# Kernel tuning notes

Hardware: AMD Instinct MI355X
Metric: run time of the kernel (lower is better)

## Reference

```python
import jax, jax.numpy as jnp
import numpy as np
from jax import lax

B, T, H, E, V = 1000, 101, 256, 256, 64


def _lstm(x, Wih, Whh, bih, bhh):
    # x: [B, T, D_in]; PyTorch gate order i, f, g, o. Initial hidden/cell are zeros.
    Bx = x.shape[0]
    Hh = Whh.shape[1]
    b = bih + bhh
    h0 = jnp.zeros((Bx, Hh), x.dtype)
    c0 = jnp.zeros((Bx, Hh), x.dtype)

    def step(carry, xt):
        h, c = carry
        g = xt @ Wih.T + h @ Whh.T + b  # [B, 4H]
        i, f, gg, o = jnp.split(g, 4, axis=-1)
        c = jax.nn.sigmoid(f) * c + jax.nn.sigmoid(i) * jnp.tanh(gg)
        h = jax.nn.sigmoid(o) * jnp.tanh(c)
        return (h, c), h

    _, hs = lax.scan(step, (h0, c0), jnp.swapaxes(x, 0, 1))  # hs: [T, B, H]
    return jnp.swapaxes(hs, 0, 1)


def setup_inputs():
    key = jax.random.key(0)
    ks = jax.random.split(key, 20)
    n = lambda k, s: jax.random.normal(k, s, jnp.float32) * 0.05
    return {
        'input_ids': jax.random.randint(ks[0], (B, T), 0, V, dtype=jnp.int32),
        'emb': n(ks[1], (V, E)),
        'Wih1': n(ks[2], (4 * H, E)), 'Whh1': n(ks[3], (4 * H, H)),
        'bih1': n(ks[4], (4 * H,)), 'bhh1': n(ks[5], (4 * H,)),
        'Wih2': n(ks[6], (4 * H, H)), 'Whh2': n(ks[7], (4 * H, H)),
        'bih2': n(ks[8], (4 * H,)), 'bhh2': n(ks[9], (4 * H,)),
        'Wattn': n(ks[10], (T, H, H)), 'battn': n(ks[11], (T, H)),
        'W1': n(ks[12], (512, H * T)), 'b1': n(ks[13], (512,)),
        'W2': n(ks[14], (128, 512)), 'b2': n(ks[15], (128,)),
        'W3': n(ks[16], (64, 128)), 'b3': n(ks[17], (64,)),
        'Wout': n(ks[18], (1, 64)), 'bout': n(ks[19], (1,)),
    }


def reference(input_ids, emb, Wih1, Whh1, bih1, bhh1, Wih2, Whh2, bih2, bhh2,
              Wattn, battn, W1, b1, W2, b2, W3, b3, Wout, bout):
    x = emb[input_ids]                                    # [B, T, E]
    h1 = _lstm(x, Wih1, Whh1, bih1, bhh1)                 # [B, T, H]
    h2 = _lstm(h1, Wih2, Whh2, bih2, bhh2)                # [B, T, H]
    # per-timestep Linear (the 101-call loop in torch), fused as one batched GEMM
    attn = jnp.einsum('bth,tkh->btk', h2, Wattn) + battn  # y_t = h_t @ W_t.T + b_t
    w = jax.nn.softmax(attn, axis=2)                      # softmax over feature dim
    applied = w * x                                       # [B, T, E]
    flat = applied.reshape(applied.shape[0], -1)          # [B, T*E]
    d = jax.nn.relu(flat @ W1.T + b1)
    d = jax.nn.relu(d @ W2.T + b2)
    d = jax.nn.relu(d @ W3.T + b3)
    tag = d @ Wout.T + bout                               # [B, 1]
    return tag, applied
```

## Files before the change

kernel.cpp:

```cpp
#include <hip/hip_runtime.h>
#include <hip/hip_bf16.h>


#define B_    1000
#define T_    101
#define E_    256
#define H_    256
#define BPAD  1008
#define MPAD  101824
#define NG    1024
#define NSLICE 63

typedef __bf16 bf16;
typedef __bf16 bf16x8 __attribute__((ext_vector_type(8)));
typedef float  f32x4  __attribute__((ext_vector_type(4)));

__device__ __forceinline__ bf16 f2b(float f){
  unsigned u = __builtin_bit_cast(unsigned, f);
  u += 0x7FFFu + ((u >> 16) & 1u);
  unsigned short h = (unsigned short)(u >> 16);
  return __builtin_bit_cast(bf16, h);
}
__device__ __forceinline__ unsigned packbf(float a, float b){
  unsigned ua = __builtin_bit_cast(unsigned, a);
  ua += 0x7FFFu + ((ua >> 16) & 1u);
  unsigned ub = __builtin_bit_cast(unsigned, b);
  ub += 0x7FFFu + ((ub >> 16) & 1u);
  return (ua >> 16) | (ub & 0xffff0000u);
}
__device__ __forceinline__ float sigm(float x){ return 1.f/(1.f + __expf(-x)); }
__device__ __forceinline__ float tanh_(float x){ return 2.f/(1.f + __expf(-2.f*x)) - 1.f; }

__global__ void pack_bT(const float* __restrict__ src, bf16* __restrict__ dst,
                        int N, int K)
{
  const long batch = blockIdx.y;
  src += batch * (long)N * K;
  dst += batch * (long)(K/32) * N * 32;
  const int tid = blockIdx.x * blockDim.x + threadIdx.x;
  const int total = (K/32) * N * 4;
  if (tid >= total) return;
  const int kkc = tid & 3;
  const int rem = tid >> 2;
  const int n = rem % N;
  const int q = rem / N;
  const float* s = src + (long)n*K + q*32 + kkc*8;
  bf16x8 v;
  #pragma unroll
  for (int e=0;e<8;e++) v[e] = f2b(s[e]);
  *reinterpret_cast<bf16x8*>(dst + ((long)q*N + n)*32 + kkc*8) = v;
}

__global__ void tr_f32(const float* __restrict__ src, float* __restrict__ dst,
                       int N, int K)
{
  const int id = blockIdx.x * blockDim.x + threadIdx.x;
  if (id >= N*K) return;
  const int k = id / N, j = id % N;
  dst[(long)k*N + j] = src[(long)j*K + k];
}

__global__ void bias_sum(const float* __restrict__ a, const float* __restrict__ b,
                         float* __restrict__ o, int n)
{
  const int i = blockIdx.x * blockDim.x + threadIdx.x;
  if (i < n) o[i] = a[i] + b[i];
}

__global__ void embed_k(const int* __restrict__ ids, const float* __restrict__ emb,
                        bf16* __restrict__ x)
{
  const int tid = blockIdx.x * blockDim.x + threadIdx.x;
  const int m = tid >> 5;
  const int c = (tid & 31) << 3;
  bf16x8 v;
  if (m < B_*T_) {
    const int id = ids[m];
    const float* e = emb + (long)id*E_ + c;
    #pragma unroll
    for (int j=0;j<8;j++) v[j] = f2b(e[j]);
  } else {
    #pragma unroll
    for (int j=0;j<8;j++) v[j] = f2b(0.f);
  }
  *reinterpret_cast<bf16x8*>(x + (long)m*256 + c) = v;
}

#define MF(a,b,c) __builtin_amdgcn_mfma_f32_16x16x32_bf16((a),(b),(c),0,0,0)
#define LDW(q_,off_)  (*reinterpret_cast<const bf16x8*>(bbW + ((long)(q_)*NG + (off_))*32))
#define LDX8(q_,off_) (*reinterpret_cast<const bf16x8*>(bbX + ((long)(q_)*NG + (off_))*32))

#define XK_ALL() { \
  bf16x8 xA0 = LDX8(0,0), xA1 = LDX8(0,16), xB0, xB1; \
  _Pragma("unroll") \
  for (int h2x=0; h2x<4; ++h2x){ \
    const int q0x = 2*h2x; \
    xB0 = LDX8(q0x+1,0); xB1 = LDX8(q0x+1,16); \
    { bf16x8 ax = *reinterpret_cast<const bf16x8*>(&xbuf[l16*264 + q0x*32 + lg*8]); \
      acc0 = MF(ax,xA0,acc0); acc1 = MF(ax,xA1,acc1); } \
    if (q0x+2 < 8){ xA0 = LDX8(q0x+2,0); xA1 = LDX8(q0x+2,16); } \
    { bf16x8 ax = *reinterpret_cast<const bf16x8*>(&xbuf[l16*264 + (q0x+1)*32 + lg*8]); \
      acc0 = MF(ax,xB0,acc0); acc1 = MF(ax,xB1,acc1); } \
  } }

__launch_bounds__(512, 1)
__global__ void lstm_v4(const bf16* __restrict__ X, const bf16* __restrict__ Wihp,
                        const bf16* __restrict__ Whhp, const float* __restrict__ bias,
                        bf16* __restrict__ Hout, unsigned* __restrict__ hX,
                        unsigned* __restrict__ flags)
{
  __shared__ __align__(16) bf16 hbuf[16*264];
  __shared__ __align__(16) bf16 xbuf[16*264];
  __shared__ float gstage[256*17];
  const int bid = blockIdx.x;
  const int s = bid >> 2, g = bid & 3;
  const int b0 = s * 16;
  const int tid = threadIdx.x;
  const int wave = tid >> 6, lane = tid & 63;
  const int l16 = lane & 15, lg = lane >> 4;
  const int qd  = wave >> 1;
  const int h32 = (wave & 1) * 32;

  const bf16* bbW = Whhp + ((long)(qd*256 + g*64 + h32 + l16) * 32 + lg*8);
  const bf16* bbX = Wihp + ((long)(qd*256 + g*64 + h32 + l16) * 32 + lg*8);

  const int row = tid >> 5;
  const int k32 = tid & 31;
  const int j2  = k32 * 2;
  float c0 = 0.f, c1 = 0.f;

  const long grow = (long)(b0 + row) * T_;
  const bf16* xp  = X    + grow*256 + k32*8;
  bf16*       hop = Hout + grow*256 + g*64 + j2;

  const float bvi0 = bias[      g*64 + j2    ];
  const float bvi1 = bias[      g*64 + j2 + 1];
  const float bvf0 = bias[256 + g*64 + j2    ];
  const float bvf1 = bias[256 + g*64 + j2 + 1];
  const float bvg0 = bias[512 + g*64 + j2    ];
  const float bvg1 = bias[512 + g*64 + j2 + 1];
  const float bvo0 = bias[768 + g*64 + j2    ];
  const float bvo1 = bias[768 + g*64 + j2 + 1];

  unsigned* flag = flags + s*16;
  unsigned* hx0 = hX + (size_t)s*2048 + row*128 + g*32 + k32;
  unsigned* hx1 = hx0 + (size_t)NSLICE*2048;
  const unsigned* rb0 = hX + (size_t)s*2048 + row*128;
  const unsigned* rb1 = rb0 + (size_t)NSLICE*2048;

  const int qo0 = 2*g, qo1 = 2*g + 1;

  for (int i = tid; i < 16*264; i += 512) hbuf[i] = f2b(0.f);
  *reinterpret_cast<bf16x8*>(&xbuf[row*264 + k32*8]) =
      *reinterpret_cast<const bf16x8*>(xp);
  __syncthreads();

  bf16x8 f0[6], f1[6];
  #pragma unroll
  for (int i=0;i<6;++i){
    const int qn = (qo0 + 2 + i) & 7;
    f0[i] = LDW(qn, 0);
    f1[i] = LDW(qn, 16);
  }
  const bf16x8 o00 = LDW(qo0, 0), o01 = LDW(qo0, 16);
  const bf16x8 o10 = LDW(qo1, 0), o11 = LDW(qo1, 16);

  f32x4 acc0 = {0.f,0.f,0.f,0.f}, acc1 = {0.f,0.f,0.f,0.f};
  XK_ALL();

  for (int t = 0; t < T_; ++t){
    const bf16x8 xreg = *reinterpret_cast<const bf16x8*>(xp + (long)(t+1)*256);

    #pragma unroll
    for (int i = 0; i < 6; ++i){
      const int qi = (qo0 + 2 + i) & 7;
      bf16x8 a = *reinterpret_cast<const bf16x8*>(&hbuf[l16*264 + qi*32 + lg*8]);
      acc0 = MF(a, f0[i], acc0);
      acc1 = MF(a, f1[i], acc1);
    }
    {
      const int jj = wave*32 + l16;
      float* gc0 = &gstage[jj*17 + lg*4];
      gc0[0]=acc0[0]; gc0[1]=acc0[1]; gc0[2]=acc0[2]; gc0[3]=acc0[3];
      float* gc1 = &gstage[(jj+16)*17 + lg*4];
      gc1[0]=acc1[0]; gc1[1]=acc1[1]; gc1[2]=acc1[2]; gc1[3]=acc1[3];
    }
    __syncthreads();

    const float i0 = sigm (bvi0 + gstage[(j2      )*17 + row]);
    const float i1 = sigm (bvi1 + gstage[(j2 +   1)*17 + row]);
    const float f0e= sigm (bvf0 + gstage[(j2 +  64)*17 + row]);
    const float f1e= sigm (bvf1 + gstage[(j2 +  65)*17 + row]);
    const float g0e= tanh_(bvg0 + gstage[(j2 + 128)*17 + row]);
    const float g1e= tanh_(bvg1 + gstage[(j2 + 129)*17 + row]);
    const float o0 = sigm (bvo0 + gstage[(j2 + 192)*17 + row]);
    const float o1 = sigm (bvo1 + gstage[(j2 + 193)*17 + row]);
    c0 = f0e*c0 + i0*g0e;
    c1 = f1e*c1 + i1*g1e;
    const unsigned hw = packbf(o0*tanh_(c0), o1*tanh_(c1));

    *reinterpret_cast<unsigned*>(&hbuf[row*264 + g*64 + j2]) = hw;
    *reinterpret_cast<bf16x8*>(&xbuf[row*264 + k32*8]) = xreg;
    __hip_atomic_store((t&1) ? hx1 : hx0, hw, __ATOMIC_RELAXED, __HIP_MEMORY_SCOPE_AGENT);

    __syncthreads();
    if (tid == 0)
      __hip_atomic_fetch_add(flag, 1u, __ATOMIC_RELAXED, __HIP_MEMORY_SCOPE_AGENT);

    *reinterpret_cast<unsigned*>(hop + (long)t*256) = hw;

    {
      acc0 = f32x4{0.f,0.f,0.f,0.f};
      acc1 = f32x4{0.f,0.f,0.f,0.f};
      bf16x8 a0 = *reinterpret_cast<const bf16x8*>(&hbuf[l16*264 + qo0*32 + lg*8]);
      acc0 = MF(a0, o00, acc0); acc1 = MF(a0, o01, acc1);
      bf16x8 a1 = *reinterpret_cast<const bf16x8*>(&hbuf[l16*264 + qo1*32 + lg*8]);
      acc0 = MF(a1, o10, acc0); acc1 = MF(a1, o11, acc1);
      XK_ALL();
    }

    {
      const unsigned tgt = 4u*(t+1);
      if (lane == 0){
        int guard = 0;
        while (__hip_atomic_load(flag, __ATOMIC_RELAXED, __HIP_MEMORY_SCOPE_AGENT) < tgt
               && ++guard < (1<<20))
          __builtin_amdgcn_s_sleep(1);
      }
      asm volatile("" ::: "memory");
      __builtin_amdgcn_sched_barrier(0);
      const unsigned* rb = (t&1) ? rb1 : rb0;
      #pragma unroll
      for (int sb=1; sb<4; ++sb){
        const int g2 = (g + sb) & 3;
        const unsigned w = __hip_atomic_load(rb + g2*32 + k32,
                                             __ATOMIC_RELAXED, __HIP_MEMORY_SCOPE_AGENT);
        *reinterpret_cast<unsigned*>(&hbuf[row*264 + g2*64 + j2]) = w;
      }
    }
    __syncthreads();
  }
}

__launch_bounds__(256)
__global__ void attn_applied(const bf16* __restrict__ H2, const bf16* __restrict__ Wap,
                             const float* __restrict__ battn, const int* __restrict__ ids,
                             const float* __restrict__ emb, float* __restrict__ applied,
                             bf16* __restrict__ flat)
{
  __shared__ __align__(16) bf16 albuf[32*264];
  __shared__ float sbuf[32*257];
  const int mt = blockIdx.x, t = blockIdx.y;
  const int b0 = mt*32;
  const int tid = threadIdx.x;
  const int wave = tid >> 6, lane = tid & 63;
  const int l16 = lane & 15, lg = lane >> 4;

  for (int i = tid; i < 1024; i += 256){
    const int r = i >> 5, cc = (i & 31) << 3;
    const int b = b0 + r;
    bf16x8 v;
    if (b < B_) v = *reinterpret_cast<const bf16x8*>(H2 + ((long)b*T_ + t)*256 + cc);
    else { 
      #pragma unroll
      for (int j=0;j<8;j++) v[j] = f2b(0.f);
    }
    *reinterpret_cast<bf16x8*>(&albuf[r*264 + cc]) = v;
  }
  __syncthreads();

  f32x4 acc[2][4];
  #pragma unroll
  for (int ms=0; ms<2; ++ms)
    #pragma unroll
    for (int ns=0; ns<4; ++ns) acc[ms][ns] = f32x4{0.f,0.f,0.f,0.f};

  const bf16* bb = Wap + (long)t*65536 + ((long)(wave*64 + l16) * 32 + lg*8);
  #pragma unroll 2
  for (int q=0; q<8; ++q){
    bf16x8 a0 = *reinterpret_cast<const bf16x8*>(&albuf[l16*264 + q*32 + lg*8]);
    bf16x8 a1 = *reinterpret_cast<const bf16x8*>(&albuf[(16 + l16)*264 + q*32 + lg*8]);
    #pragma unroll
    for (int ns=0; ns<4; ++ns){
      bf16x8 b = *reinterpret_cast<const bf16x8*>(bb + ((long)q*256 + ns*16) * 32);
      acc[0][ns] = __builtin_amdgcn_mfma_f32_16x16x32_bf16(a0, b, acc[0][ns], 0,0,0);
      acc[1][ns] = __builtin_amdgcn_mfma_f32_16x16x32_bf16(a1, b, acc[1][ns], 0,0,0);
    }
  }
  float bv[4];
  #pragma unroll
  for (int ns=0; ns<4; ++ns) bv[ns] = battn[t*256 + wave*64 + ns*16 + l16];
  #pragma unroll
  for (int ms=0; ms<2; ++ms)
    #pragma unroll
    for (int ns=0; ns<4; ++ns)
      #pragma unroll
      for (int r=0; r<4; ++r)
        sbuf[(ms*16 + lg*4 + r)*257 + wave*64 + ns*16 + l16] = acc[ms][ns][r] + bv[ns];
  __syncthreads();

  const int row = tid >> 3, seg = tid & 7;
  const float* srow = &sbuf[row*257 + seg*32];
  float v[32];
  float mx = -1e30f;
  #pragma unroll
  for (int i=0;i<32;++i){ v[i] = srow[i]; mx = fmaxf(mx, v[i]); }
  #pragma unroll
  for (int off=1; off<8; off<<=1) mx = fmaxf(mx, __shfl_xor(mx, off));
  float s = 0.f;
  #pragma unroll
  for (int i=0;i<32;++i){ v[i] = __expf(v[i] - mx); s += v[i]; }
  #pragma unroll
  for (int off=1; off<8; off<<=1) s += __shfl_xor(s, off);
  const float inv = 1.f / s;
  const int b = b0 + row;
  if (b < B_){
    const int id = ids[b*T_ + t];
    const float* ex = emb + (long)id*256 + seg*32;
    float* ap = applied + ((long)b*T_ + t)*256 + seg*32;
    bf16* fp = flat + (long)b*25856 + t*256 + seg*32;
    #pragma unroll
    for (int i=0;i<32;++i){
      const float val = v[i]*inv*ex[i];
      ap[i] = val;
      fp[i] = f2b(val);
    }
  }
}

__launch_bounds__(512)
__global__ void gemm_mlp1(const bf16* __restrict__ A, const bf16* __restrict__ Bp,
                          float* __restrict__ part)
{
  const int m0 = blockIdx.x * 32;
  const int ks = blockIdx.y;
  const int tid = threadIdx.x;
  const int wave = tid >> 6, lane = tid & 63;
  const int l16 = lane & 15, lg = lane >> 4;
  f32x4 acc[2][4];
  #pragma unroll
  for (int ms=0; ms<2; ++ms)
    #pragma unroll
    for (int ns=0; ns<4; ++ns) acc[ms][ns] = f32x4{0.f,0.f,0.f,0.f};

  const bf16* arow0 = A + (long)(m0 + l16)*25856 + lg*8;
  const bf16* arow1 = A + (long)(m0 + 16 + l16)*25856 + lg*8;
  const bf16* bb = Bp + ((long)(wave*64 + l16) * 32 + lg*8);
  #pragma unroll 2
  for (int q = ks*101; q < ks*101 + 101; ++q){
    bf16x8 a0 = *reinterpret_cast<const bf16x8*>(arow0 + (long)q*32);
    bf16x8 a1 = *reinterpret_cast<const bf16x8*>(arow1 + (long)q*32);
    #pragma unroll
    for (int ns=0; ns<4; ++ns){
      bf16x8 b = *reinterpret_cast<const bf16x8*>(bb + ((long)q*512 + ns*16) * 32);
      acc[0][ns] = __builtin_amdgcn_mfma_f32_16x16x32_bf16(a0, b, acc[0][ns], 0,0,0);
      acc[1][ns] = __builtin_amdgcn_mfma_f32_16x16x32_bf16(a1, b, acc[1][ns], 0,0,0);
    }
  }
  #pragma unroll
  for (int ms=0; ms<2; ++ms)
    #pragma unroll
    for (int ns=0; ns<4; ++ns)
      #pragma unroll
      for (int r=0; r<4; ++r)
        part[((long)ks*1024 + m0 + ms*16 + lg*4 + r)*512 + wave*64 + ns*16 + l16] = acc[ms][ns][r];
}

__global__ void reduce_relu(const float* __restrict__ part, const float* __restrict__ b1,
                            float* __restrict__ d1)
{
  const int idx = blockIdx.x*256 + threadIdx.x;
  const int n = idx & 511, m = idx >> 9;
  float s = b1[n];
  #pragma unroll
  for (int k=0;k<8;k++) s += part[((long)k*1024 + m)*512 + n];
  d1[idx] = fmaxf(s, 0.f);
}

__launch_bounds__(128)
__global__ void mlp_tail(const float* __restrict__ d1, const float* __restrict__ W2T,
                         const float* __restrict__ b2, const float* __restrict__ W3T,
                         const float* __restrict__ b3, const float* __restrict__ Wout,
                         const float* __restrict__ bout, float* __restrict__ tag)
{
  __shared__ float r1[512];
  __shared__ float r2[128];
  __shared__ float r3[64];
  const int b = blockIdx.x;
  const int tid = threadIdx.x;
  for (int i = tid; i < 512; i += 128) r1[i] = d1[(long)b*512 + i];
  __syncthreads();
  float a = b2[tid];
  #pragma unroll 8
  for (int k=0;k<512;++k) a += W2T[k*128 + tid] * r1[k];
  r2[tid] = fmaxf(a, 0.f);
  __syncthreads();
  if (tid < 64){
    float a3 = b3[tid];
    #pragma unroll 8
    for (int k=0;k<128;++k) a3 += W3T[k*64 + tid] * r2[k];
    r3[tid] = fmaxf(a3, 0.f);
  }
  __syncthreads();
  if (tid < 64){
    float p = r3[tid] * Wout[tid];
    #pragma unroll
    for (int off=1; off<64; off<<=1) p += __shfl_xor(p, off);
    if (tid == 0) tag[b] = p + bout[0];
  }
}

extern "C" void kernel_launch(void* const* d_in, const int* in_sizes, int n_in,
                              void* d_out, int out_size, void* d_ws, size_t ws_size,
                              hipStream_t stream)
{
  const int*   ids   = (const int*)  d_in[0];
  const float* emb   = (const float*)d_in[1];
  const float* Wih1  = (const float*)d_in[2];
  const float* Whh1  = (const float*)d_in[3];
  const float* bih1  = (const float*)d_in[4];
  const float* bhh1  = (const float*)d_in[5];
  const float* Wih2  = (const float*)d_in[6];
  const float* Whh2  = (const float*)d_in[7];
  const float* bih2  = (const float*)d_in[8];
  const float* bhh2  = (const float*)d_in[9];
  const float* Wattn = (const float*)d_in[10];
  const float* battn = (const float*)d_in[11];
  const float* W1    = (const float*)d_in[12];
  const float* b1    = (const float*)d_in[13];
  const float* W2    = (const float*)d_in[14];
  const float* b2    = (const float*)d_in[15];
  const float* W3    = (const float*)d_in[16];
  const float* b3    = (const float*)d_in[17];
  const float* Wout  = (const float*)d_in[18];
  const float* bout  = (const float*)d_in[19];
  float* out = (float*)d_out;
  char*  ws  = (char*)d_ws;

  constexpr size_t OW_IH1 = 0;
  constexpr size_t OW_HH1 = 524288;
  constexpr size_t OW_IH2 = 1048576;
  constexpr size_t OW_HH2 = 1572864;
  constexpr size_t OW_ATT = 2097152;
  constexpr size_t OW_W1  = 15335424;
  constexpr size_t OW_W2T = 41811968;
  constexpr size_t OW_W3T = 42074112;
  constexpr size_t OB1    = 42106880;
  constexpr size_t OB2    = 42110976;
  constexpr size_t OXH2   = 42115072;
  constexpr size_t OG     = 94248960;
  constexpr size_t OFLAT  = OG;
  constexpr size_t OPART  = OG + 52953088;
  constexpr size_t OH1    = 302784512;
  constexpr size_t OD1    = 354918400;
  constexpr size_t OHX    = OD1;
  constexpr size_t OFLG   = OD1 + 1032192;
  constexpr size_t NEED   = 357015552;
  if (ws_size < NEED) return;

  bf16*  pIH1 = (bf16*) (ws + OW_IH1);
  bf16*  pHH1 = (bf16*) (ws + OW_HH1);
  bf16*  pIH2 = (bf16*) (ws + OW_IH2);
  bf16*  pHH2 = (bf16*) (ws + OW_HH2);
  bf16*  pATT = (bf16*) (ws + OW_ATT);
  bf16*  pW1  = (bf16*) (ws + OW_W1);
  float* pW2T = (float*)(ws + OW_W2T);
  float* pW3T = (float*)(ws + OW_W3T);
  float* pB1  = (float*)(ws + OB1);
  float* pB2  = (float*)(ws + OB2);
  bf16*  pXH2 = (bf16*) (ws + OXH2);
  bf16*  pFLAT= (bf16*) (ws + OFLAT);
  float* pPART= (float*)(ws + OPART);
  bf16*  pH1  = (bf16*) (ws + OH1);
  float* pD1  = (float*)(ws + OD1);
  unsigned* pHX  = (unsigned*)(ws + OHX);
  unsigned* pFL1 = (unsigned*)(ws + OFLG);
  unsigned* pFL2 = (unsigned*)(ws + OFLG + 4096);

  hipMemsetAsync(ws + OFLG, 0, 8192, stream);
  hipMemsetAsync(ws + OFLAT + (size_t)B_*25856*2, 0, (size_t)24*25856*2, stream);

  pack_bT<<<dim3(128),        256, 0, stream>>>(Wih1,  pIH1, 1024, 256);
  pack_bT<<<dim3(128),        256, 0, stream>>>(Whh1,  pHH1, 1024, 256);
  pack_bT<<<dim3(128),        256, 0, stream>>>(Wih2,  pIH2, 1024, 256);
  pack_bT<<<dim3(128),        256, 0, stream>>>(Whh2,  pHH2, 1024, 256);
  pack_bT<<<dim3(32, 101),    256, 0, stream>>>(Wattn, pATT, 256,  256);
  pack_bT<<<dim3(6464),       256, 0, stream>>>(W1,    pW1,  512,  25856);
  tr_f32 <<<dim3(256),        256, 0, stream>>>(W2, pW2T, 128, 512);
  tr_f32 <<<dim3(32),         256, 0, stream>>>(W3, pW3T, 64, 128);
  bias_sum<<<dim3(4),         256, 0, stream>>>(bih1, bhh1, pB1, 1024);
  bias_sum<<<dim3(4),         256, 0, stream>>>(bih2, bhh2, pB2, 1024);

  embed_k<<<dim3(12728), 256, 0, stream>>>(ids, emb, pXH2);

  lstm_v4<<<dim3(252), 512, 0, stream>>>(pXH2, pIH1, pHH1, pB1, pH1,  pHX, pFL1);
  lstm_v4<<<dim3(252), 512, 0, stream>>>(pH1,  pIH2, pHH2, pB2, pXH2, pHX, pFL2);

  attn_applied<<<dim3(32, 101), 256, 0, stream>>>(pXH2, pATT, battn, ids, emb,
                                                  out + 1000, pFLAT);

  gemm_mlp1  <<<dim3(32, 8), 512, 0, stream>>>(pFLAT, pW1, pPART);
  reduce_relu<<<dim3(2048),  256, 0, stream>>>(pPART, b1, pD1);
  mlp_tail   <<<dim3(1000),  128, 0, stream>>>(pD1, pW2T, b2, pW3T, b3, Wout, bout, out);
}
```

Measured before the change: 870.2 us.

## Use per-group step flags in LSTM, reload weights per step, remap grids for XCD locality

The LSTM's single atomic counter per batch slice, bumped by fetch_add, becomes four per-group flags, each written with a plain atomic store and polled together, so the atomic read-modify-write on a shared counter goes away. The own-slice Whh fragments and the f0/f1 weight registers are now reloaded from global memory every step instead of held for the whole kernel, which lowers register pressure but adds a load per step. The attn_applied and gemm_mlp1 launches switch to 1D grids whose block index is decoded so blocks that share data land on the same XCD, aiming for better L2 reuse. The extra per-step weight loads could lengthen the serial LSTM critical path.

```diff
diff --git a/kernel.cpp b/kernel.cpp
--- a/kernel.cpp
+++ b/kernel.cpp
@@ -104,7 +104,7 @@
   } }
 
 __launch_bounds__(512, 1)
-__global__ void lstm_v4(const bf16* __restrict__ X, const bf16* __restrict__ Wihp,
+__global__ void lstm_v5(const bf16* __restrict__ X, const bf16* __restrict__ Wihp,
                         const bf16* __restrict__ Whhp, const float* __restrict__ bias,
                         bf16* __restrict__ Hout, unsigned* __restrict__ hX,
                         unsigned* __restrict__ flags)
@@ -142,7 +142,7 @@
   const float bvo0 = bias[768 + g*64 + j2    ];
   const float bvo1 = bias[768 + g*64 + j2 + 1];
 
-  unsigned* flag = flags + s*16;
+  unsigned* flagw = flags + s*16;
   unsigned* hx0 = hX + (size_t)s*2048 + row*128 + g*32 + k32;
   unsigned* hx1 = hx0 + (size_t)NSLICE*2048;
   const unsigned* rb0 = hX + (size_t)s*2048 + row*128;
@@ -162,8 +162,6 @@
     f0[i] = LDW(qn, 0);
     f1[i] = LDW(qn, 16);
   }
-  const bf16x8 o00 = LDW(qo0, 0), o01 = LDW(qo0, 16);
-  const bf16x8 o10 = LDW(qo1, 0), o11 = LDW(qo1, 16);
 
   f32x4 acc0 = {0.f,0.f,0.f,0.f}, acc1 = {0.f,0.f,0.f,0.f};
   XK_ALL();
@@ -205,11 +203,14 @@
 
     __syncthreads();
     if (tid == 0)
-      __hip_atomic_fetch_add(flag, 1u, __ATOMIC_RELAXED, __HIP_MEMORY_SCOPE_AGENT);
+      __hip_atomic_store(flagw + g, (unsigned)(t+1),
+                         __ATOMIC_RELAXED, __HIP_MEMORY_SCOPE_AGENT);
 
     *reinterpret_cast<unsigned*>(hop + (long)t*256) = hw;
 
     {
+      bf16x8 o00 = LDW(qo0, 0), o01 = LDW(qo0, 16);
+      bf16x8 o10 = LDW(qo1, 0), o11 = LDW(qo1, 16);
       acc0 = f32x4{0.f,0.f,0.f,0.f};
       acc1 = f32x4{0.f,0.f,0.f,0.f};
       bf16x8 a0 = *reinterpret_cast<const bf16x8*>(&hbuf[l16*264 + qo0*32 + lg*8]);
@@ -217,15 +218,27 @@
       bf16x8 a1 = *reinterpret_cast<const bf16x8*>(&hbuf[l16*264 + qo1*32 + lg*8]);
       acc0 = MF(a1, o10, acc0); acc1 = MF(a1, o11, acc1);
       XK_ALL();
+      #pragma unroll
+      for (int i=0;i<6;++i){
+        const int qn = (qo0 + 2 + i) & 7;
+        f0[i] = LDW(qn, 0);
+        f1[i] = LDW(qn, 16);
+      }
     }
 
     {
-      const unsigned tgt = 4u*(t+1);
+      const unsigned tgt = (unsigned)(t+1);
       if (lane == 0){
         int guard = 0;
-        while (__hip_atomic_load(flag, __ATOMIC_RELAXED, __HIP_MEMORY_SCOPE_AGENT) < tgt
-               && ++guard < (1<<20))
+        for (;;){
+          const unsigned a0 = __hip_atomic_load(flagw+0, __ATOMIC_RELAXED, __HIP_MEMORY_SCOPE_AGENT);
+          const unsigned a1 = __hip_atomic_load(flagw+1, __ATOMIC_RELAXED, __HIP_MEMORY_SCOPE_AGENT);
+          const unsigned a2 = __hip_atomic_load(flagw+2, __ATOMIC_RELAXED, __HIP_MEMORY_SCOPE_AGENT);
+          const unsigned a3 = __hip_atomic_load(flagw+3, __ATOMIC_RELAXED, __HIP_MEMORY_SCOPE_AGENT);
+          if ((a0 >= tgt) & (a1 >= tgt) & (a2 >= tgt) & (a3 >= tgt)) break;
+          if (++guard >= (1<<20)) break;
           __builtin_amdgcn_s_sleep(1);
+        }
       }
       asm volatile("" ::: "memory");
       __builtin_amdgcn_sched_barrier(0);
@@ -250,7 +263,12 @@
 {
   __shared__ __align__(16) bf16 albuf[32*264];
   __shared__ float sbuf[32*257];
-  const int mt = blockIdx.x, t = blockIdx.y;
+  const int bid = blockIdx.x;
+  const int xcd = bid & 7;
+  const int qq  = bid >> 3;
+  const int t   = xcd + 8*(qq % 13);
+  const int mt  = qq / 13;
+  if (t >= T_) return;
   const int b0 = mt*32;
   const int tid = threadIdx.x;
   const int wave = tid >> 6, lane = tid & 63;
@@ -332,8 +350,8 @@
 __global__ void gemm_mlp1(const bf16* __restrict__ A, const bf16* __restrict__ Bp,
                           float* __restrict__ part)
 {
-  const int m0 = blockIdx.x * 32;
-  const int ks = blockIdx.y;
+  const int ks = blockIdx.x & 7;
+  const int m0 = (blockIdx.x >> 3) * 32;
   const int tid = threadIdx.x;
   const int wave = tid >> 6, lane = tid & 63;
   const int l16 = lane & 15, lg = lane >> 4;
@@ -493,13 +511,13 @@
 
   embed_k<<<dim3(12728), 256, 0, stream>>>(ids, emb, pXH2);
 
-  lstm_v4<<<dim3(252), 512, 0, stream>>>(pXH2, pIH1, pHH1, pB1, pH1,  pHX, pFL1);
-  lstm_v4<<<dim3(252), 512, 0, stream>>>(pH1,  pIH2, pHH2, pB2, pXH2, pHX, pFL2);
-
-  attn_applied<<<dim3(32, 101), 256, 0, stream>>>(pXH2, pATT, battn, ids, emb,
-                                                  out + 1000, pFLAT);
-
-  gemm_mlp1  <<<dim3(32, 8), 512, 0, stream>>>(pFLAT, pW1, pPART);
-  reduce_relu<<<dim3(2048),  256, 0, stream>>>(pPART, b1, pD1);
-  mlp_tail   <<<dim3(1000),  128, 0, stream>>>(pD1, pW2T, b2, pW3T, b3, Wout, bout, out);
-}
+  lstm_v5<<<dim3(252), 512, 0, stream>>>(pXH2, pIH1, pHH1, pB1, pH1,  pHX, pFL1);
+  lstm_v5<<<dim3(252), 512, 0, stream>>>(pH1,  pIH2, pHH2, pB2, pXH2, pHX, pFL2);
+
+  attn_applied<<<dim3(3328), 256, 0, stream>>>(pXH2, pATT, battn, ids, emb,
+                                               out + 1000, pFLAT);
+
+  gemm_mlp1  <<<dim3(256),  512, 0, stream>>>(pFLAT, pW1, pPART);
+  reduce_relu<<<dim3(2048), 256, 0, stream>>>(pPART, b1, pD1);
+  mlp_tail   <<<dim3(1000), 128, 0, stream>>>(pD1, pW2T, b2, pW3T, b3, Wout, bout, out);
+}
```

Measured after the change: 877.4 us. About the same (+0.8%).
